# Optimization experiments

Measured on AMD Instinct MI355X. Metric: run time of the kernel, lower is better.

The kernel has to match this reference:

```python
import jax, jax.numpy as jnp
from jax import lax
import numpy as np

B, C_IN, IMG = 128, 3, 64
NH, D, K = 128, 256, 1024
BETA = 0.1        # beta buffer initialized to beta_start
BA_ITERS = 5
EPS = 1e-10


def _conv(x, w, b, stride, pad):
    y = lax.conv_general_dilated(x, w, (stride, stride), ((pad, pad), (pad, pad)),
                                 dimension_numbers=("NCHW", "OIHW", "NCHW"))
    return y + b[None, :, None, None]


def _convT(x, w, b):
    # PyTorch ConvTranspose2d(k=4, s=2, p=1); w: [Cin, Cout, 4, 4]
    wt = jnp.flip(w, (2, 3)).transpose(1, 0, 2, 3)  # -> [Cout, Cin, 4, 4]
    y = lax.conv_general_dilated(x, wt, (1, 1), ((2, 2), (2, 2)),
                                 lhs_dilation=(2, 2),
                                 dimension_numbers=("NCHW", "OIHW", "NCHW"))
    return y + b[None, :, None, None]


def _res(x, w1, b1, w2, b2):
    h = jax.nn.relu(_conv(x, w1, b1, 1, 1))
    h = _conv(h, w2, b2, 1, 1)
    return jax.nn.relu(h + x)


def setup_inputs() -> dict:
    key = jax.random.key(0)
    ks = iter(jax.random.split(key, 40))

    def w(shape):
        fan_in = int(np.prod(shape[1:]))
        return jax.random.normal(next(ks), shape, jnp.float32) / np.float32(np.sqrt(fan_in))

    z = lambda n: jnp.zeros((n,), jnp.float32)
    inp = {"x": jax.random.normal(next(ks), (B, C_IN, IMG, IMG), jnp.float32)}
    inp.update(
        ew1=w((NH, 3, 4, 4)), eb1=z(NH),
        ew2=w((2 * NH, NH, 4, 4)), eb2=z(2 * NH),
        ew3=w((D, 2 * NH, 3, 3)), eb3=z(D),
        er1aw=w((D, D, 3, 3)), er1ab=z(D), er1bw=w((D, D, 3, 3)), er1bb=z(D),
        er2aw=w((D, D, 3, 3)), er2ab=z(D), er2bw=w((D, D, 3, 3)), er2bb=z(D),
        codebook=jax.random.uniform(next(ks), (K, D), jnp.float32, -1.0 / K, 1.0 / K),
        pi=jnp.full((K,), 1.0 / K, jnp.float32),
        dr1aw=w((D, D, 3, 3)), dr1ab=z(D), dr1bw=w((D, D, 3, 3)), dr1bb=z(D),
        dr2aw=w((D, D, 3, 3)), dr2ab=z(D), dr2bw=w((D, D, 3, 3)), dr2bb=z(D),
        dw1=w((2 * NH, D, 3, 3)), db1=z(2 * NH),
        dwt2=w((2 * NH, NH, 4, 4)), dbt2=z(NH),
        dwt3=w((NH, 3, 4, 4)), dbt3=z(3),
    )
    return inp


def reference(x, ew1, eb1, ew2, eb2, ew3, eb3,
              er1aw, er1ab, er1bw, er1bb, er2aw, er2ab, er2bw, er2bb,
              codebook, pi,
              dr1aw, dr1ab, dr1bw, dr1bb, dr2aw, dr2ab, dr2bw, dr2bb,
              dw1, db1, dwt2, dbt2, dwt3, dbt3):
    # ---- encoder: [B,3,H,W] -> [B,D,H/4,W/4] ----
    h = jax.nn.relu(_conv(x, ew1, eb1, 2, 1))
    h = jax.nn.relu(_conv(h, ew2, eb2, 2, 1))
    h = jax.nn.relu(_conv(h, ew3, eb3, 1, 1))
    h = _res(h, er1aw, er1ab, er1bw, er1bb)
    z = _res(h, er2aw, er2ab, er2bw, er2bb)

    Bn, Dn, Hl, Wl = z.shape
    zf = z.transpose(0, 2, 3, 1).reshape(-1, Dn)  # [N, D]

    # squared euclidean distances [N, K]
    d = (jnp.sum(zf * zf, axis=1, keepdims=True)
         + jnp.sum(codebook * codebook, axis=1)
         - 2.0 * (zf @ codebook.T))

    # ---- Blahut-Arimoto iterations ----
    Q = pi
    for _ in range(BA_ITERS):
        logits = jnp.log(jnp.clip(Q, EPS)) - BETA * d  # [N, K]
        P = jax.nn.softmax(logits, axis=1)
        Q = jnp.clip(jnp.mean(P, axis=0), EPS)

    zq_soft = P @ codebook                              # [N, D]
    idx = jnp.argmax(P, axis=1)

    commit = 0.25 * jnp.mean((zf - lax.stop_gradient(zq_soft)) ** 2)
    cb_loss = jnp.mean((zq_soft - lax.stop_gradient(zf)) ** 2)
    ent = -jnp.sum(Q * jnp.log(jnp.clip(Q, EPS)))
    ent_loss = -0.01 * ent

    zq_hard = codebook[idx]
    zq = zq_soft + lax.stop_gradient(zq_hard - zq_soft)  # straight-through
    zq = zq.reshape(Bn, Hl, Wl, Dn).transpose(0, 3, 1, 2)

    # ---- decoder ----
    h = _res(zq, dr1aw, dr1ab, dr1bw, dr1bb)
    h = _res(h, dr2aw, dr2ab, dr2bw, dr2bb)
    h = jax.nn.relu(_conv(h, dw1, db1, 1, 1))
    h = jax.nn.relu(_convT(h, dwt2, dbt2))
    x_recon = _convT(h, dwt3, dbt3)
    return x_recon, commit, cb_loss, ent_loss
```

## Files before the change

kernel.cpp:

```cpp
#include <hip/hip_runtime.h>
#include <math.h>

#define NB   128
#define DC   256
#define SP   256
#define NROW 32768
#define KCB  1024
#define BETA_F 0.1f
#define EPSQ 1e-10f

typedef __attribute__((ext_vector_type(8))) short s16x8;
typedef __attribute__((ext_vector_type(4))) short s16x4;
typedef __attribute__((ext_vector_type(4))) float f32x4;

__device__ __forceinline__ short f2bf(float f) {
  unsigned u = __builtin_bit_cast(unsigned, f);
  unsigned r = (u + 0x7FFFu + ((u >> 16) & 1u)) >> 16;
  return (short)r;
}
__device__ __forceinline__ float bf2f(short s) {
  unsigned u = ((unsigned)(unsigned short)s) << 16;
  return __builtin_bit_cast(float, u);
}
__device__ __forceinline__ unsigned pack2(float a, float b) {
  return (unsigned)(unsigned short)f2bf(a) | ((unsigned)(unsigned short)f2bf(b) << 16);
}

__global__ void init0_kernel(short* __restrict__ zerob)
{
  if (threadIdx.x < 8) zerob[threadIdx.x] = 0;
}

__global__ void w3t_kernel(const float* __restrict__ w, short* __restrict__ o)
{
  const int i = blockIdx.x * 256 + threadIdx.x;
  const int ci = i & 255, co = (i >> 8) & 255, j = i >> 16;
  o[i] = f2bf(w[((size_t)(co * 256 + ci)) * 9 + j]);
}
__global__ void w2t_kernel(const float* __restrict__ w, short* __restrict__ o)
{
  const int i = blockIdx.x * 256 + threadIdx.x;
  const int ci = i & 127, co = (i >> 7) & 255, j = i >> 15;
  o[i] = f2bf(w[((size_t)(co * 128 + ci)) * 16 + j]);
}
__global__ void wtt2_kernel(const float* __restrict__ w, short* __restrict__ o)
{
  const int i = blockIdx.x * 256 + threadIdx.x;
  const int ci = i & 255, co = (i >> 8) & 127, j = (i >> 15) & 3, p = i >> 17;
  const int po = p >> 1, pq = p & 1, a = j >> 1, b2 = j & 1;
  const int kh = (1 - po) + 2 * a, kw = (1 - pq) + 2 * b2;
  o[i] = f2bf(w[((size_t)(ci * 128 + co)) * 16 + kh * 4 + kw]);
}
__global__ void cbbf_kernel(const float* __restrict__ cb, short* __restrict__ o)
{
  const int i = blockIdx.x * 256 + threadIdx.x;
  o[i] = f2bf(cb[i]);
}
__global__ void cbt_kernel(const float* __restrict__ cb, short* __restrict__ o)
{
  const int i = blockIdx.x * 256 + threadIdx.x;
  const int d = i >> 10, k = i & 1023;
  o[i] = f2bf(cb[(size_t)k * 256 + d]);
}

__global__ __launch_bounds__(256) void conv1_kernel(
    const float* __restrict__ x, const float* __restrict__ w,
    const float* __restrict__ bias, short* __restrict__ out)
{
  __shared__ float li[3][34][34];
  const int tid = threadIdx.x;
  const int tile = blockIdx.x;
  const int b = blockIdx.y;
  const int qy = tile >> 1, qx = tile & 1;
  const int ihlo = qy * 32 - 1, iwlo = qx * 32 - 1;
  for (int ci = 0; ci < 3; ++ci)
    for (int s = tid; s < 1156; s += 256) {
      const int r = s / 34, c = s - r * 34;
      const int ih = ihlo + r, iw = iwlo + c;
      float v = 0.f;
      if ((unsigned)ih < 64u && (unsigned)iw < 64u)
        v = x[((size_t)(b * 3 + ci) * 64 + ih) * 64 + iw];
      li[ci][r][c] = v;
    }
  __syncthreads();

  const int wv = tid >> 6, l = tid & 63;
  const int co0 = 2 * l, co1 = 2 * l + 1;
  float w0[48], w1[48];
#pragma unroll
  for (int j = 0; j < 48; ++j) {
    w0[j] = w[(size_t)co0 * 48 + j];
    w1[j] = w[(size_t)co1 * 48 + j];
  }
  const float b0 = bias[co0], b1 = bias[co1];

  for (int pass = 0; pass < 64; ++pass) {
    const int pix = pass * 4 + wv;
    const int py = pix >> 4, px = pix & 15;
    float s0 = b0, s1 = b1;
#pragma unroll
    for (int ci = 0; ci < 3; ++ci)
#pragma unroll
      for (int kh = 0; kh < 4; ++kh)
#pragma unroll
        for (int kw = 0; kw < 4; ++kw) {
          const int j = ci * 16 + kh * 4 + kw;
          const float v = li[ci][2 * py + kh][2 * px + kw];
          s0 = fmaf(v, w0[j], s0);
          s1 = fmaf(v, w1[j], s1);
        }
    s0 = fmaxf(s0, 0.f);
    s1 = fmaxf(s1, 0.f);
    const int oh = qy * 16 + py, ow = qx * 16 + px;
    ((unsigned*)(out + ((size_t)b * 1024 + oh * 32 + ow) * 128))[l] = pack2(s0, s1);
  }
}

template<int MODE, int KIT, int AK, int KPN, int TS>
__global__ __launch_bounds__(256) void igemm_kernel(
    const short* __restrict__ Abuf, const short* __restrict__ Bw,
    const float* __restrict__ bias, const short* __restrict__ res,
    short* __restrict__ outb, float* __restrict__ outf32,
    float* __restrict__ sacc, const short* __restrict__ zerob)
{
  __shared__ __align__(16) short Alds[2][8192];
  __shared__ float red[4];
  const int tid = threadIdx.x;
  const int wv = tid >> 6, l = tid & 63;
  const int wm = wv >> 1, wn = wv & 1;
  const int lcol = l & 15, lk = l >> 4;
  const int m0 = blockIdx.x * 128;

  int ncol0 = 0, po = 0, pq = 0;
  const short* Bp = Bw;
  if constexpr (MODE == 3) {
    po = blockIdx.y >> 1; pq = blockIdx.y & 1;
    Bp += (size_t)blockIdx.y * 131072;
  } else {
    ncol0 = blockIdx.y * 128;
    Bp += (size_t)ncol0 * KPN;
  }

  const int cpos = l & 3;
  const int rl_[2] = { (wv * 2) * 16 + (l >> 2), (wv * 2 + 1) * 16 + (l >> 2) };
  const int cc_[2] = { cpos ^ ((rl_[0] >> 1) & 3), cpos ^ ((rl_[1] >> 1) & 3) };

  f32x4 acc[4][4];
#pragma unroll
  for (int i = 0; i < 4; ++i)
#pragma unroll
    for (int j = 0; j < 4; ++j) acc[i][j] = (f32x4){0.f, 0.f, 0.f, 0.f};

  const int aoff_base = lcol * 32 + ((lk ^ ((lcol >> 1) & 3)) * 8);

  auto STAGE = [&](int it, int bufc) {
    int jj, kk;
    if constexpr (MODE == 0 || MODE == 3) { jj = it >> 3; kk = it & 7; }
    else if constexpr (MODE == 2)         { jj = it >> 2; kk = it & 3; }
    else                                  { jj = 0; kk = it; }
    const int choff = kk * 32;
    (void)jj;
#pragma unroll
    for (int q = 0; q < 2; ++q) {
      const int rl = rl_[q], cc = cc_[q];
      const int m = m0 + rl;
      const short* srcA;
      if constexpr (MODE == 0) {
        const int q3 = jj / 3;
        const int ih = ((m >> 4) & 15) + q3 - 1, iw = (m & 15) + (jj - q3 * 3) - 1;
        const bool v = ((unsigned)ih < 16u) & ((unsigned)iw < 16u);
        srcA = v ? Abuf + (size_t)((m & ~255) + ih * 16 + iw) * AK + choff + cc * 8 : zerob;
      } else if constexpr (MODE == 2) {
        const int ih = 2 * ((m >> 4) & 15) + (jj >> 2) - 1, iw = 2 * (m & 15) + (jj & 3) - 1;
        const bool v = ((unsigned)ih < 32u) & ((unsigned)iw < 32u);
        srcA = v ? Abuf + (size_t)((m >> 8) * 1024 + ih * 32 + iw) * AK + choff + cc * 8 : zerob;
      } else if constexpr (MODE == 3) {
        const int ih = ((m >> 4) & 15) + po - (jj >> 1), iw = (m & 15) + pq - (jj & 1);
        const bool v = ((unsigned)ih < 16u) & ((unsigned)iw < 16u);
        srcA = v ? Abuf + (size_t)((m & ~255) + ih * 16 + iw) * AK + choff + cc * 8 : zerob;
      } else {
        srcA = Abuf + (size_t)m * AK + choff + cc * 8;
      }
      __builtin_amdgcn_global_load_lds(
          (const __attribute__((address_space(1))) void*)srcA,
          (__attribute__((address_space(3))) void*)(&Alds[bufc][(wv * 2 + q) * 512]),
          16, 0, 0);
      const short* srcB = Bp + (size_t)jj * TS + (size_t)rl * KPN + choff + cc * 8;
      __builtin_amdgcn_global_load_lds(
          (const __attribute__((address_space(1))) void*)srcB,
          (__attribute__((address_space(3))) void*)(&Alds[bufc][4096 + (wv * 2 + q) * 512]),
          16, 0, 0);
    }
  };

  auto COMPUTE = [&](int it, int bufc) {
    (void)it;
    s16x8 a[4], b[4];
#pragma unroll
    for (int ms = 0; ms < 4; ++ms)
      a[ms] = *(const s16x8*)&Alds[bufc][wm * 2048 + ms * 512 + aoff_base];
#pragma unroll
    for (int ns = 0; ns < 4; ++ns)
      b[ns] = *(const s16x8*)&Alds[bufc][4096 + wn * 2048 + ns * 512 + aoff_base];
#pragma unroll
    for (int ms = 0; ms < 4; ++ms)
#pragma unroll
      for (int ns = 0; ns < 4; ++ns)
        acc[ms][ns] = __builtin_amdgcn_mfma_f32_16x16x32_bf16(a[ms], b[ns], acc[ms][ns], 0, 0, 0);
  };

  STAGE(0, 0);
  for (int it = 0; it < KIT; it += 2) {
    __syncthreads();
    if (it + 1 < KIT) STAGE(it + 1, 1);
    COMPUTE(it, 0);
    __syncthreads();
    if (it + 2 < KIT) STAGE(it + 2, 0);
    COMPUTE(it + 1, 1);
  }

  const int r4 = lk * 4;
  float ls = 0.f;
#pragma unroll
  for (int ms = 0; ms < 4; ++ms) {
#pragma unroll
    for (int ns = 0; ns < 4; ++ns) {
      const int n_l = wn * 64 + ns * 16 + lcol;
      const int n_g = ncol0 + n_l;
#pragma unroll
      for (int e = 0; e < 4; ++e) {
        const int m = m0 + wm * 64 + ms * 16 + r4 + e;
        if constexpr (MODE == 4) {
          const float val = bias[n_g] - 2.f * acc[ms][ns][e];
          outb[(size_t)m * 1024 + n_g] = f2bf(val);
        } else if constexpr (MODE == 5) {
          const float d = acc[ms][ns][e] - outf32[(size_t)m * 256 + n_g];
          ls = fmaf(d, d, ls);
        } else if constexpr (MODE == 3) {
          const float val = fmaxf(acc[ms][ns][e] + bias[n_l], 0.f);
          const int orow = (m & ~255) * 4 + (2 * ((m >> 4) & 15) + po) * 32 + (2 * (m & 15) + pq);
          outb[(size_t)orow * 128 + n_l] = f2bf(val);
        } else {
          float val = acc[ms][ns][e] + bias[n_g];
          if (res) val += bf2f(res[(size_t)m * 256 + n_g]);
          val = fmaxf(val, 0.f);
          outb[(size_t)m * 256 + n_g] = f2bf(val);
          if (outf32) outf32[(size_t)m * 256 + n_g] = val;
        }
      }
    }
  }
  if constexpr (MODE == 5) {
#pragma unroll
    for (int o = 32; o > 0; o >>= 1) ls += __shfl_xor(ls, o);
    if (l == 0) red[wv] = ls;
    __syncthreads();
    if (tid == 0) atomicAdd(sacc, red[0] + red[1] + red[2] + red[3]);
  }
}

__global__ __launch_bounds__(256) void rownorm_kernel(
    const float* __restrict__ a, float* __restrict__ nrm, int rows)
{
  const int wv = threadIdx.x >> 6, lane = threadIdx.x & 63;
  const int r = blockIdx.x * 4 + wv;
  if (r >= rows) return;
  const float* p = a + (size_t)r * DC;
  float s = 0.f;
#pragma unroll
  for (int i = 0; i < 4; ++i) { float v = p[lane + 64 * i]; s = fmaf(v, v, s); }
#pragma unroll
  for (int o = 32; o > 0; o >>= 1) s += __shfl_xor(s, o);
  if (lane == 0) nrm[r] = s;
}

__global__ void initq_kernel(const float* __restrict__ pi, float* __restrict__ logq,
                             float* __restrict__ Sacc)
{
  const int k = blockIdx.x * 256 + threadIdx.x;
  logq[k] = logf(fmaxf(pi[k], EPSQ));
  if (k == 0) *Sacc = 0.f;
}

__global__ __launch_bounds__(256) void ba2_kernel(
    uint4* __restrict__ DV, const float* __restrict__ logq,
    float* __restrict__ part, int* __restrict__ idxout, int storeP)
{
  __shared__ float qp[4][1024];
  const int tid = threadIdx.x;
  const int wv = tid >> 6, lane = tid & 63;

  float lq[16];
  {
    const float4* lq4 = (const float4*)logq;
#pragma unroll
    for (int h = 0; h < 2; ++h) {
      const float4 a = lq4[h * 128 + 2 * lane];
      const float4 b = lq4[h * 128 + 2 * lane + 1];
      lq[h * 8 + 0] = a.x; lq[h * 8 + 1] = a.y; lq[h * 8 + 2] = a.z; lq[h * 8 + 3] = a.w;
      lq[h * 8 + 4] = b.x; lq[h * 8 + 5] = b.y; lq[h * 8 + 6] = b.z; lq[h * 8 + 7] = b.w;
    }
  }

  float qacc[16];
#pragma unroll
  for (int j = 0; j < 16; ++j) qacc[j] = 0.f;

  const int n0 = blockIdx.x * 16;
  for (int rr = 0; rr < 4; ++rr) {
    const int n = n0 + wv * 4 + rr;
    uint4* rowp = DV + (size_t)n * 128;
    uint4 w[2];
    w[0] = rowp[lane];
    w[1] = rowp[64 + lane];
    float lv[16];
    float mx = -1e30f;
#pragma unroll
    for (int h = 0; h < 2; ++h) {
      const unsigned* u = (const unsigned*)&w[h];
#pragma unroll
      for (int p = 0; p < 4; ++p) {
        lv[h * 8 + 2 * p]     = lq[h * 8 + 2 * p]     - BETA_F * bf2f((short)(u[p] & 0xFFFFu));
        lv[h * 8 + 2 * p + 1] = lq[h * 8 + 2 * p + 1] - BETA_F * bf2f((short)(u[p] >> 16));
      }
    }
#pragma unroll
    for (int j = 0; j < 16; ++j) mx = fmaxf(mx, lv[j]);
#pragma unroll
    for (int o = 32; o > 0; o >>= 1) mx = fmaxf(mx, __shfl_xor(mx, o));
    float e[16];
    float s = 0.f;
#pragma unroll
    for (int j = 0; j < 16; ++j) { e[j] = __expf(lv[j] - mx); s += e[j]; }
#pragma unroll
    for (int o = 32; o > 0; o >>= 1) s += __shfl_xor(s, o);
    const float inv = 1.f / s;
#pragma unroll
    for (int j = 0; j < 16; ++j) qacc[j] += e[j] * inv;

    if (storeP) {
#pragma unroll
      for (int h = 0; h < 2; ++h) {
        unsigned* u = (unsigned*)&w[h];
#pragma unroll
        for (int p = 0; p < 4; ++p)
          u[p] = pack2(e[h * 8 + 2 * p] * inv, e[h * 8 + 2 * p + 1] * inv);
      }
      rowp[lane] = w[0];
      rowp[64 + lane] = w[1];
      float bv = lv[0]; int bi = 8 * lane;
#pragma unroll
      for (int h = 0; h < 2; ++h)
#pragma unroll
        for (int j = 0; j < 8; ++j) {
          const int k = h * 512 + 8 * lane + j;
          const float v = lv[h * 8 + j];
          if (v > bv || (v == bv && k < bi)) { bv = v; bi = k; }
        }
#pragma unroll
      for (int o = 32; o > 0; o >>= 1) {
        const float ov = __shfl_xor(bv, o);
        const int oi = __shfl_xor(bi, o);
        if (ov > bv || (ov == bv && oi < bi)) { bv = ov; bi = oi; }
      }
      if (lane == 0) idxout[n] = bi;
    }
  }
  __syncthreads();
#pragma unroll
  for (int h = 0; h < 2; ++h)
#pragma unroll
    for (int j = 0; j < 8; ++j)
      qp[wv][h * 512 + 8 * lane + j] = qacc[h * 8 + j];
  __syncthreads();
  for (int k = tid; k < 1024; k += 256) {
    part[(size_t)blockIdx.x * 1024 + k] = qp[0][k] + qp[1][k] + qp[2][k] + qp[3][k];
  }
}

__global__ __launch_bounds__(256) void qred1_kernel(
    const float* __restrict__ part, float* __restrict__ part2)
{
  const int b = blockIdx.x;
  const int tid = threadIdx.x;
  const float* p = part + (size_t)b * 32 * 1024;
#pragma unroll
  for (int j = 0; j < 4; ++j) {
    const int k = tid + j * 256;
    float s = 0.f;
#pragma unroll
    for (int r = 0; r < 32; ++r) s += p[(size_t)r * 1024 + k];
    part2[(size_t)b * 1024 + k] = s;
  }
}

__global__ __launch_bounds__(256) void qred2_kernel(
    const float* __restrict__ part2, float* __restrict__ qsum, float* __restrict__ logq)
{
  const int k = blockIdx.x * 256 + threadIdx.x;
  float s = 0.f;
#pragma unroll
  for (int r = 0; r < 64; ++r) s += part2[(size_t)r * 1024 + k];
  qsum[k] = s;
  logq[k] = logf(fmaxf(s * (1.f / 32768.f), EPSQ));
}

__global__ __launch_bounds__(1024) void ent_kernel(
    const float* __restrict__ qsum, float* __restrict__ out_ent)
{
  const int k = threadIdx.x;
  const float q = fmaxf(qsum[k] * (1.f / 32768.f), EPSQ);
  float v = q * logf(q);
#pragma unroll
  for (int o = 32; o > 0; o >>= 1) v += __shfl_xor(v, o);
  __shared__ float red[16];
  const int wv = k >> 6, lane = k & 63;
  if (lane == 0) red[wv] = v;
  __syncthreads();
  if (k == 0) {
    float s = 0.f;
    for (int i = 0; i < 16; ++i) s += red[i];
    *out_ent = 0.01f * s;
  }
}

__global__ void scalars_kernel(const float* __restrict__ S, float* __restrict__ out2)
{
  const float s = *S;
  out2[0] = 0.25f * s / 8388608.f;
  out2[1] = s / 8388608.f;
}

__global__ void gather16_kernel(const int* __restrict__ idx, const short* __restrict__ cbb,
                                short* __restrict__ out)
{
  const int t = blockIdx.x * 256 + threadIdx.x;
  const int m = t >> 6, d4 = (t & 63) * 4;
  *(s16x4*)(out + (size_t)m * 256 + d4) = *(const s16x4*)(cbb + (size_t)idx[m] * 256 + d4);
}

__global__ __launch_bounds__(256) void convt3_kernel(
    const short* __restrict__ in, const float* __restrict__ w,
    const float* __restrict__ bias, float* __restrict__ out)
{
  __shared__ __align__(16) short li[100 * 128];
  __shared__ float lw[6144];
  const int tid = threadIdx.x;
  const int tile = blockIdx.x;
  const int b = blockIdx.y;
  const int ty0 = (tile >> 2) * 16, tx0 = (tile & 3) * 16;
  const int iy0 = (tile >> 2) * 8 - 1, ix0 = (tile & 3) * 8 - 1;
  for (int s = tid; s < 1600; s += 256) {
    const int pix = s >> 4, ch = s & 15;
    const int r = pix / 10, c = pix - r * 10;
    const int ih = iy0 + r, iw = ix0 + c;
    s16x8 v = {0, 0, 0, 0, 0, 0, 0, 0};
    if ((unsigned)ih < 32u && (unsigned)iw < 32u)
      v = *(const s16x8*)(in + ((size_t)b * 1024 + ih * 32 + iw) * 128 + ch * 8);
    const int slot = ch ^ (pix & 15);
    *(s16x8*)&li[pix * 128 + slot * 8] = v;
  }
  for (int s = tid; s < 6144; s += 256) lw[s] = w[s];
  __syncthreads();
  const int ty = tid >> 4, tx = tid & 15;
  const int oh2 = ty0 + ty, ow2 = tx0 + tx;
  const int kh0 = (oh2 + 1) & 1, kw0 = (ow2 + 1) & 1;
  const int ih0 = (oh2 + 1 - kh0) >> 1, iw0 = (ow2 + 1 - kw0) >> 1;
  const int rl0 = ih0 - iy0, cl0 = iw0 - ix0;
  const int p00 = rl0 * 10 + cl0, p01 = p00 - 1, p10 = p00 - 10, p11 = p00 - 11;
  const int wi00 = kh0 * 4 + kw0, wi01 = wi00 + 2, wi10 = wi00 + 8, wi11 = wi00 + 10;
  float acc0 = 0.f, acc1 = 0.f, acc2 = 0.f;
  for (int ch = 0; ch < 16; ++ch) {
    const s16x8 v00 = *(const s16x8*)&li[p00 * 128 + (ch ^ (p00 & 15)) * 8];
    const s16x8 v01 = *(const s16x8*)&li[p01 * 128 + (ch ^ (p01 & 15)) * 8];
    const s16x8 v10 = *(const s16x8*)&li[p10 * 128 + (ch ^ (p10 & 15)) * 8];
    const s16x8 v11 = *(const s16x8*)&li[p11 * 128 + (ch ^ (p11 & 15)) * 8];
#pragma unroll
    for (int e = 0; e < 8; ++e) {
      const int ci = ch * 8 + e;
      const float* wr = &lw[ci * 48];
      const float f00 = bf2f(v00[e]), f01 = bf2f(v01[e]);
      const float f10 = bf2f(v10[e]), f11 = bf2f(v11[e]);
      acc0 = fmaf(wr[wi00], f00, fmaf(wr[wi01], f01, fmaf(wr[wi10], f10, fmaf(wr[wi11], f11, acc0))));
      acc1 = fmaf(wr[16 + wi00], f00, fmaf(wr[16 + wi01], f01, fmaf(wr[16 + wi10], f10, fmaf(wr[16 + wi11], f11, acc1))));
      acc2 = fmaf(wr[32 + wi00], f00, fmaf(wr[32 + wi01], f01, fmaf(wr[32 + wi10], f10, fmaf(wr[32 + wi11], f11, acc2))));
    }
  }
  const size_t ob = ((size_t)(b * 3) * 64 + oh2) * 64 + ow2;
  out[ob] = acc0 + bias[0];
  out[ob + 4096] = acc1 + bias[1];
  out[ob + 8192] = acc2 + bias[2];
}

extern "C" void kernel_launch(void* const* d_in, const int* in_sizes, int n_in,
                              void* d_out, int out_size, void* d_ws, size_t ws_size,
                              hipStream_t stream)
{
  const float* x     = (const float*)d_in[0];
  const float* ew1   = (const float*)d_in[1];
  const float* eb1   = (const float*)d_in[2];
  const float* ew2   = (const float*)d_in[3];
  const float* eb2   = (const float*)d_in[4];
  const float* ew3   = (const float*)d_in[5];
  const float* eb3   = (const float*)d_in[6];
  const float* er1aw = (const float*)d_in[7];
  const float* er1ab = (const float*)d_in[8];
  const float* er1bw = (const float*)d_in[9];
  const float* er1bb = (const float*)d_in[10];
  const float* er2aw = (const float*)d_in[11];
  const float* er2ab = (const float*)d_in[12];
  const float* er2bw = (const float*)d_in[13];
  const float* er2bb = (const float*)d_in[14];
  const float* cb    = (const float*)d_in[15];
  const float* pi    = (const float*)d_in[16];
  const float* dr1aw = (const float*)d_in[17];
  const float* dr1ab = (const float*)d_in[18];
  const float* dr1bw = (const float*)d_in[19];
  const float* dr1bb = (const float*)d_in[20];
  const float* dr2aw = (const float*)d_in[21];
  const float* dr2ab = (const float*)d_in[22];
  const float* dr2bw = (const float*)d_in[23];
  const float* dr2bb = (const float*)d_in[24];
  const float* dw1   = (const float*)d_in[25];
  const float* db1   = (const float*)d_in[26];
  const float* dwt2  = (const float*)d_in[27];
  const float* dbt2  = (const float*)d_in[28];
  const float* dwt3  = (const float*)d_in[29];
  const float* dbt3  = (const float*)d_in[30];

  float* outf = (float*)d_out;

  char* W = (char*)d_ws;
  short* BIGA  = (short*)W;
  float* ZF32  = (float*)W;
  short* DV    = (short*)(W + 33554432);
  short* X0    = (short*)(W + 100663296);
  short* X1    = (short*)(W + 117440512);
  short* X2    = (short*)(W + 134217728);
  short* WT3   = (short*)(W + 150994944);
  short* WT2   = (short*)(W + 152174592);
  short* WTT2  = (short*)(W + 153223168);
  short* CBB   = (short*)(W + 154271744);
  short* CBT   = (short*)(W + 154796032);
  float* cn    = (float*)(W + 155320320);
  float* qsum  = (float*)(W + 155324416);
  float* logq  = (float*)(W + 155328512);
  int*   idx   = (int*)(W + 155332608);
  float* Sacc  = (float*)(W + 155463680);
  short* zerob = (short*)(W + 155463696);
  float* PART  = (float*)(W + 160000000);
  float* PART2 = (float*)(W + 168388608);

  const dim3 blk(256);
  #define IG3(A_, W_, B_, R_, O_, F_) \
    igemm_kernel<0,72,256,256,65536><<<dim3(256, 2), blk, 0, stream>>>( \
        A_, W_, B_, R_, O_, F_, nullptr, zerob)

  init0_kernel<<<dim3(1), dim3(64), 0, stream>>>(zerob);

  conv1_kernel<<<dim3(4, NB), blk, 0, stream>>>(x, ew1, eb1, BIGA);
  w2t_kernel<<<dim3(2048), blk, 0, stream>>>(ew2, WT2);
  igemm_kernel<2,64,128,128,32768><<<dim3(256, 2), blk, 0, stream>>>(
      BIGA, WT2, eb2, nullptr, X0, nullptr, nullptr, zerob);
  w3t_kernel<<<dim3(2304), blk, 0, stream>>>(ew3, WT3);
  IG3(X0, WT3, eb3, nullptr, X1, nullptr);
  w3t_kernel<<<dim3(2304), blk, 0, stream>>>(er1aw, WT3);
  IG3(X1, WT3, er1ab, nullptr, X2, nullptr);
  w3t_kernel<<<dim3(2304), blk, 0, stream>>>(er1bw, WT3);
  IG3(X2, WT3, er1bb, X1, X0, nullptr);
  w3t_kernel<<<dim3(2304), blk, 0, stream>>>(er2aw, WT3);
  IG3(X0, WT3, er2ab, nullptr, X1, nullptr);
  w3t_kernel<<<dim3(2304), blk, 0, stream>>>(er2bw, WT3);
  IG3(X1, WT3, er2bb, X0, X2, ZF32);

  rownorm_kernel<<<dim3(KCB / 4), blk, 0, stream>>>(cb, cn, KCB);
  cbbf_kernel<<<dim3(1024), blk, 0, stream>>>(cb, CBB);
  cbt_kernel<<<dim3(1024), blk, 0, stream>>>(cb, CBT);
  initq_kernel<<<dim3(4), blk, 0, stream>>>(pi, logq, Sacc);
  igemm_kernel<4,8,256,256,0><<<dim3(256, 8), blk, 0, stream>>>(
      X2, CBB, cn, nullptr, DV, nullptr, nullptr, zerob);
  for (int i = 0; i < 5; ++i) {
    ba2_kernel<<<dim3(NROW / 16), blk, 0, stream>>>(
        (uint4*)DV, logq, PART, idx, (i == 4) ? 1 : 0);
    qred1_kernel<<<dim3(64), blk, 0, stream>>>(PART, PART2);
    qred2_kernel<<<dim3(4), blk, 0, stream>>>(PART2, qsum, logq);
  }
  ent_kernel<<<dim3(1), dim3(1024), 0, stream>>>(qsum, outf + 1572866);
  igemm_kernel<5,32,1024,1024,0><<<dim3(256, 2), blk, 0, stream>>>(
      DV, CBT, nullptr, nullptr, nullptr, ZF32, Sacc, zerob);
  scalars_kernel<<<dim3(1), dim3(1), 0, stream>>>(Sacc, outf + 1572864);
  gather16_kernel<<<dim3(8192), blk, 0, stream>>>(idx, CBB, X0);

  w3t_kernel<<<dim3(2304), blk, 0, stream>>>(dr1aw, WT3);
  IG3(X0, WT3, dr1ab, nullptr, X1, nullptr);
  w3t_kernel<<<dim3(2304), blk, 0, stream>>>(dr1bw, WT3);
  IG3(X1, WT3, dr1bb, X0, X2, nullptr);
  w3t_kernel<<<dim3(2304), blk, 0, stream>>>(dr2aw, WT3);
  IG3(X2, WT3, dr2ab, nullptr, X0, nullptr);
  w3t_kernel<<<dim3(2304), blk, 0, stream>>>(dr2bw, WT3);
  IG3(X0, WT3, dr2bb, X2, X1, nullptr);
  w3t_kernel<<<dim3(2304), blk, 0, stream>>>(dw1, WT3);
  IG3(X1, WT3, db1, nullptr, X0, nullptr);
  wtt2_kernel<<<dim3(2048), blk, 0, stream>>>(dwt2, WTT2);
  igemm_kernel<3,32,256,256,32768><<<dim3(256, 4), blk, 0, stream>>>(
      X0, WTT2, dbt2, nullptr, BIGA, nullptr, nullptr, zerob);
  convt3_kernel<<<dim3(16, NB), blk, 0, stream>>>(BIGA, dwt3, dbt3, outf);
  #undef IG3
}
```

Baseline: 1.006 ms.

## Triple-buffer igemm LDS pipeline and batch all 3x3 weight transposes into one launch

The implicit-GEMM main loop moves from a double buffer with two __syncthreads per iteration pair to a three-stage LDS ring. It waits on vmcnt for the stage in flight, uses one barrier per iteration, and raises wave priority around the MFMA compute. The goal is to hide global-to-LDS load latency behind more compute. Separately, the ten 3x3 weight transposes are merged into one 2D-grid kernel writing distinct slabs, which removes nine launches and the serialization between each transpose and its conv. The cost is more LDS per block (48KB instead of 32KB), which may lower occupancy, and the hand-coded vmcnt count depends on the number of loads each STAGE issues.

```diff
diff --git a/kernel.cpp b/kernel.cpp
--- a/kernel.cpp
+++ b/kernel.cpp
@@ -31,11 +31,19 @@
   if (threadIdx.x < 8) zerob[threadIdx.x] = 0;
 }
 
-__global__ void w3t_kernel(const float* __restrict__ w, short* __restrict__ o)
-{
+__global__ void w3t10_kernel(
+    const float* __restrict__ w0, const float* __restrict__ w1,
+    const float* __restrict__ w2, const float* __restrict__ w3,
+    const float* __restrict__ w4, const float* __restrict__ w5,
+    const float* __restrict__ w6, const float* __restrict__ w7,
+    const float* __restrict__ w8, const float* __restrict__ w9,
+    short* __restrict__ o)
+{
+  const float* ws[10] = {w0, w1, w2, w3, w4, w5, w6, w7, w8, w9};
+  const float* w = ws[blockIdx.y];
   const int i = blockIdx.x * 256 + threadIdx.x;
   const int ci = i & 255, co = (i >> 8) & 255, j = i >> 16;
-  o[i] = f2bf(w[((size_t)(co * 256 + ci)) * 9 + j]);
+  o[(size_t)blockIdx.y * 589824 + i] = f2bf(w[((size_t)(co * 256 + ci)) * 9 + j]);
 }
 __global__ void w2t_kernel(const float* __restrict__ w, short* __restrict__ o)
 {
@@ -123,7 +131,7 @@
     short* __restrict__ outb, float* __restrict__ outf32,
     float* __restrict__ sacc, const short* __restrict__ zerob)
 {
-  __shared__ __align__(16) short Alds[2][8192];
+  __shared__ __align__(16) short Alds[3][8192];
   __shared__ float red[4];
   const int tid = threadIdx.x;
   const int wv = tid >> 6, l = tid & 63;
@@ -193,8 +201,7 @@
     }
   };
 
-  auto COMPUTE = [&](int it, int bufc) {
-    (void)it;
+  auto COMPUTE = [&](int bufc) {
     s16x8 a[4], b[4];
 #pragma unroll
     for (int ms = 0; ms < 4; ++ms)
@@ -210,13 +217,23 @@
   };
 
   STAGE(0, 0);
-  for (int it = 0; it < KIT; it += 2) {
-    __syncthreads();
-    if (it + 1 < KIT) STAGE(it + 1, 1);
-    COMPUTE(it, 0);
-    __syncthreads();
-    if (it + 2 < KIT) STAGE(it + 2, 0);
-    COMPUTE(it + 1, 1);
+  STAGE(1, 1);
+  int buf = 0, nbuf = 2;
+#pragma unroll 1
+  for (int it = 0; it < KIT; ++it) {
+    if (it + 1 < KIT) {
+      asm volatile("s_waitcnt vmcnt(4)" ::: "memory");
+    } else {
+      asm volatile("s_waitcnt vmcnt(0)" ::: "memory");
+    }
+    __builtin_amdgcn_s_barrier();
+    __builtin_amdgcn_sched_barrier(0);
+    if (it + 2 < KIT) STAGE(it + 2, nbuf);
+    __builtin_amdgcn_s_setprio(1);
+    COMPUTE(buf);
+    __builtin_amdgcn_s_setprio(0);
+    buf = (buf == 2) ? 0 : buf + 1;
+    nbuf = (nbuf == 2) ? 0 : nbuf + 1;
   }
 
   const int r4 = lk * 4;
@@ -537,7 +554,6 @@
   short* X0    = (short*)(W + 100663296);
   short* X1    = (short*)(W + 117440512);
   short* X2    = (short*)(W + 134217728);
-  short* WT3   = (short*)(W + 150994944);
   short* WT2   = (short*)(W + 152174592);
   short* WTT2  = (short*)(W + 153223168);
   short* CBB   = (short*)(W + 154271744);
@@ -550,28 +566,27 @@
   short* zerob = (short*)(W + 155463696);
   float* PART  = (float*)(W + 160000000);
   float* PART2 = (float*)(W + 168388608);
+  short* WT3S  = (short*)(W + 168650752);
 
   const dim3 blk(256);
-  #define IG3(A_, W_, B_, R_, O_, F_) \
+  #define WTSLAB(i) (WT3S + (size_t)(i) * 589824)
+  #define IG3(A_, Wi_, B_, R_, O_, F_) \
     igemm_kernel<0,72,256,256,65536><<<dim3(256, 2), blk, 0, stream>>>( \
-        A_, W_, B_, R_, O_, F_, nullptr, zerob)
+        A_, WTSLAB(Wi_), B_, R_, O_, F_, nullptr, zerob)
 
   init0_kernel<<<dim3(1), dim3(64), 0, stream>>>(zerob);
+  w3t10_kernel<<<dim3(2304, 10), blk, 0, stream>>>(
+      ew3, er1aw, er1bw, er2aw, er2bw, dr1aw, dr1bw, dr2aw, dr2bw, dw1, WT3S);
 
   conv1_kernel<<<dim3(4, NB), blk, 0, stream>>>(x, ew1, eb1, BIGA);
   w2t_kernel<<<dim3(2048), blk, 0, stream>>>(ew2, WT2);
   igemm_kernel<2,64,128,128,32768><<<dim3(256, 2), blk, 0, stream>>>(
       BIGA, WT2, eb2, nullptr, X0, nullptr, nullptr, zerob);
-  w3t_kernel<<<dim3(2304), blk, 0, stream>>>(ew3, WT3);
-  IG3(X0, WT3, eb3, nullptr, X1, nullptr);
-  w3t_kernel<<<dim3(2304), blk, 0, stream>>>(er1aw, WT3);
-  IG3(X1, WT3, er1ab, nullptr, X2, nullptr);
-  w3t_kernel<<<dim3(2304), blk, 0, stream>>>(er1bw, WT3);
-  IG3(X2, WT3, er1bb, X1, X0, nullptr);
-  w3t_kernel<<<dim3(2304), blk, 0, stream>>>(er2aw, WT3);
-  IG3(X0, WT3, er2ab, nullptr, X1, nullptr);
-  w3t_kernel<<<dim3(2304), blk, 0, stream>>>(er2bw, WT3);
-  IG3(X1, WT3, er2bb, X0, X2, ZF32);
+  IG3(X0, 0, eb3, nullptr, X1, nullptr);
+  IG3(X1, 1, er1ab, nullptr, X2, nullptr);
+  IG3(X2, 2, er1bb, X1, X0, nullptr);
+  IG3(X0, 3, er2ab, nullptr, X1, nullptr);
+  IG3(X1, 4, er2bb, X0, X2, ZF32);
 
   rownorm_kernel<<<dim3(KCB / 4), blk, 0, stream>>>(cb, cn, KCB);
   cbbf_kernel<<<dim3(1024), blk, 0, stream>>>(cb, CBB);
@@ -591,19 +606,15 @@
   scalars_kernel<<<dim3(1), dim3(1), 0, stream>>>(Sacc, outf + 1572864);
   gather16_kernel<<<dim3(8192), blk, 0, stream>>>(idx, CBB, X0);
 
-  w3t_kernel<<<dim3(2304), blk, 0, stream>>>(dr1aw, WT3);
-  IG3(X0, WT3, dr1ab, nullptr, X1, nullptr);
-  w3t_kernel<<<dim3(2304), blk, 0, stream>>>(dr1bw, WT3);
-  IG3(X1, WT3, dr1bb, X0, X2, nullptr);
-  w3t_kernel<<<dim3(2304), blk, 0, stream>>>(dr2aw, WT3);
-  IG3(X2, WT3, dr2ab, nullptr, X0, nullptr);
-  w3t_kernel<<<dim3(2304), blk, 0, stream>>>(dr2bw, WT3);
-  IG3(X0, WT3, dr2bb, X2, X1, nullptr);
-  w3t_kernel<<<dim3(2304), blk, 0, stream>>>(dw1, WT3);
-  IG3(X1, WT3, db1, nullptr, X0, nullptr);
+  IG3(X0, 5, dr1ab, nullptr, X1, nullptr);
+  IG3(X1, 6, dr1bb, X0, X2, nullptr);
+  IG3(X2, 7, dr2ab, nullptr, X0, nullptr);
+  IG3(X0, 8, dr2bb, X2, X1, nullptr);
+  IG3(X1, 9, db1, nullptr, X0, nullptr);
   wtt2_kernel<<<dim3(2048), blk, 0, stream>>>(dwt2, WTT2);
   igemm_kernel<3,32,256,256,32768><<<dim3(256, 4), blk, 0, stream>>>(
       X0, WTT2, dbt2, nullptr, BIGA, nullptr, nullptr, zerob);
   convt3_kernel<<<dim3(16, NB), blk, 0, stream>>>(BIGA, dwt3, dbt3, outf);
   #undef IG3
-}
+  #undef WTSLAB
+}
```

New measurement: 976.8 us. 1.03x faster.
